# Performance work log

Hardware: AMD Instinct MI355X
Metric: run time of the kernel (lower is better)

## Reference

```python
import jax, jax.numpy as jnp
import numpy as np

EMBED = 1024
HEAD = 64
BLOCK = 2048
B = 8


def setup_inputs() -> dict:
    key = jax.random.key(0)
    k1, k2, k3, k4 = jax.random.split(key, 4)
    inputs = jax.random.normal(k1, (B, BLOCK, EMBED), dtype=jnp.float32)
    s = 1.0 / np.sqrt(EMBED)
    Wk = jax.random.normal(k2, (EMBED, HEAD), dtype=jnp.float32) * s
    Wq = jax.random.normal(k3, (EMBED, HEAD), dtype=jnp.float32) * s
    Wv = jax.random.normal(k4, (EMBED, HEAD), dtype=jnp.float32) * s
    return {"inputs": inputs, "Wk": Wk, "Wq": Wq, "Wv": Wv}


def reference(inputs, Wk, Wq, Wv):
    # inputs: [B, T, E]; projections (bias-free Linear)
    k = inputs @ Wk  # [B, T, H]
    q = inputs @ Wq  # [B, T, H]
    v = inputs @ Wv  # [B, T, H]
    # Faithful to source: wei = k @ q^T (NOT q @ k^T)
    wei = jnp.einsum("bth,bsh->bts", k, q) * (HEAD ** -0.5)  # [B, T, T]
    T = inputs.shape[1]
    causal = jnp.tril(jnp.ones((T, T), dtype=bool))
    wei = jnp.where(causal, wei, -jnp.inf)
    wei = jax.nn.softmax(wei, axis=-1)
    out = jnp.einsum("bts,bsh->bth", wei, v)  # [B, T, H]
    return out
```

## Files before the change

### kernel.cpp

```cpp
#include <hip/hip_runtime.h>
#include <hip/hip_bf16.h>
#include <stdint.h>


typedef __attribute__((ext_vector_type(4))) float f32x4;
typedef __attribute__((ext_vector_type(4))) short s16x4;
typedef __attribute__((ext_vector_type(8))) short s16x8;
typedef __attribute__((ext_vector_type(2))) unsigned int u32x2;
typedef __attribute__((ext_vector_type(4))) unsigned int u32x4;

__device__ __forceinline__ unsigned bf16pack(float a, float b){
    unsigned ua = __builtin_bit_cast(unsigned, a);
    unsigned ub = __builtin_bit_cast(unsigned, b);
    return ((ua + 0x8000u) >> 16) | ((ub + 0x8000u) & 0xffff0000u);
}
__device__ __forceinline__ unsigned short bf16one(float a){
    return (unsigned short)((__builtin_bit_cast(unsigned, a) + 0x8000u) >> 16);
}
__device__ __forceinline__ void gload16(const void* g, unsigned short* l){
    __builtin_amdgcn_global_load_lds((const __attribute__((address_space(1))) unsigned int*)g,
                                     (__attribute__((address_space(3))) unsigned int*)l, 16, 0, 0);
}

__global__ __launch_bounds__(256) void wprep_kernel(const float* __restrict__ Wk,
                                                    const float* __restrict__ Wq,
                                                    const float* __restrict__ Wv,
                                                    unsigned short* __restrict__ WT){
    __shared__ float lw[1024][8];
    int w = blockIdx.x, n0 = blockIdx.y * 8, tid = threadIdx.x;
    const float* src = (w == 0) ? Wk : (w == 1) ? Wq : Wv;
    float scale = (w == 0) ? 0.18033688011112042f : 1.0f;
    for (int it = 0; it < 8; ++it){
        int idx = it * 256 + tid;
        int k = idx >> 1, half = idx & 1;
        f32x4 v = *(const f32x4*)(src + k * 64 + n0 + half * 4);
        *(f32x4*)&lw[k][half * 4] = v;
    }
    __syncthreads();
    int n = tid >> 5, kc = (tid & 31) * 32;
    unsigned short* dst = WT + (size_t)((w * 64 + n0 + n) * 1024 + kc);
    #pragma unroll
    for (int c = 0; c < 4; c++){
        s16x8 v;
        #pragma unroll
        for (int e = 0; e < 8; e++)
            v[e] = (short)bf16one(lw[kc + c * 8 + e][n] * scale);
        *(s16x8*)(dst + c * 8) = v;
    }
}

__global__ __launch_bounds__(256) void proj_kernel(const float* __restrict__ x,
                                                   const unsigned short* __restrict__ WT,
                                                   unsigned short* __restrict__ kb,
                                                   unsigned short* __restrict__ qb,
                                                   unsigned short* __restrict__ vT){
    __shared__ unsigned short smem[32768];
    int tid = threadIdx.x; int l = tid & 63; int w = tid >> 6;
    int lr = l & 15, lg = l >> 4;
    int row0 = blockIdx.x * 32;
    int b = row0 >> 11, t0 = row0 & 2047;
    const float* xbase = x + (size_t)row0 * 1024;

    auto stage = [&](int k0, int buf){
        #pragma unroll
        for (int t = 0; t < 2; t++){
            int i = w * 2 + t;
            int r = i * 4 + (l >> 4);
            int c = l & 15;
            gload16(xbase + (size_t)r * 1024 + k0 + ((c ^ ((r & 7) << 1)) * 4),
                    smem + buf * 4096 + i * 512);
        }
        #pragma unroll
        for (int u = 0; u < 6; u++){
            int i = w * 6 + u;
            int r = i * 8 + (l >> 3);
            int c = l & 7;
            gload16(WT + (size_t)r * 1024 + k0 + ((c ^ (r & 7)) * 8),
                    smem + 8192 + buf * 12288 + i * 512);
        }
    };

    f32x4 acc[2][3] = {};
    stage(0, 0);
    __syncthreads();
    int cur = 0;
    for (int k0 = 0; k0 < 1024; k0 += 64){
        int kn = (k0 + 64 < 1024) ? (k0 + 64) : 960;
        stage(kn, cur ^ 1);
        s16x8 af[2][2];
        #pragma unroll
        for (int mf = 0; mf < 2; mf++){
            int r = mf * 16 + lr;
            const unsigned short* xrow = smem + cur * 4096 + r * 128;
            #pragma unroll
            for (int kc = 0; kc < 2; kc++){
                int c0 = (kc * 8 + lg * 2) ^ ((r & 7) << 1);
                f32x4 v0 = *(const f32x4*)(xrow + c0 * 8);
                f32x4 v1 = *(const f32x4*)(xrow + c0 * 8 + 8);
                u32x4 pk;
                pk[0] = bf16pack(v0[0], v0[1]); pk[1] = bf16pack(v0[2], v0[3]);
                pk[2] = bf16pack(v1[0], v1[1]); pk[3] = bf16pack(v1[2], v1[3]);
                af[mf][kc] = __builtin_bit_cast(s16x8, pk);
            }
        }
        #pragma unroll
        for (int nn = 0; nn < 3; nn++){
            int r = (w * 3 + nn) * 16 + lr;
            const unsigned short* wrow = smem + 8192 + cur * 12288 + r * 64;
            s16x8 b0 = *(const s16x8*)(wrow + ((lg       ^ (r & 7)) * 8));
            s16x8 b1 = *(const s16x8*)(wrow + (((4 + lg) ^ (r & 7)) * 8));
            acc[0][nn] = __builtin_amdgcn_mfma_f32_16x16x32_bf16(af[0][0], b0, acc[0][nn], 0, 0, 0);
            acc[0][nn] = __builtin_amdgcn_mfma_f32_16x16x32_bf16(af[0][1], b1, acc[0][nn], 0, 0, 0);
            acc[1][nn] = __builtin_amdgcn_mfma_f32_16x16x32_bf16(af[1][0], b0, acc[1][nn], 0, 0, 0);
            acc[1][nn] = __builtin_amdgcn_mfma_f32_16x16x32_bf16(af[1][1], b1, acc[1][nn], 0, 0, 0);
        }
        __syncthreads();
        cur ^= 1;
    }
    #pragma unroll
    for (int mf = 0; mf < 2; mf++)
        #pragma unroll
        for (int nn = 0; nn < 3; nn++){
            int col = (w * 3 + nn) * 16 + lr;
            int row = mf * 16 + lg * 4;
            #pragma unroll
            for (int r = 0; r < 4; r++)
                smem[(row + r) * 200 + col] = bf16one(acc[mf][nn][r]);
        }
    __syncthreads();
    {
        int r2 = tid >> 3, c2 = (tid & 7) * 16;
        const unsigned short* srowp = smem + r2 * 200 + c2;
        unsigned short* dst = (c2 < 64)
            ? kb + (size_t)(b * 2048 + t0 + r2) * 64 + c2
            : qb + (size_t)(b * 2048 + t0 + r2) * 64 + (c2 - 64);
        *(s16x8*)(dst)     = *(const s16x8*)(srowp);
        *(s16x8*)(dst + 8) = *(const s16x8*)(srowp + 8);
        int h = tid >> 2, q3 = tid & 3;
        s16x8 vv;
        #pragma unroll
        for (int e = 0; e < 8; e++)
            vv[e] = smem[(q3 * 8 + e) * 200 + 128 + h];
        *(s16x8*)(vT + (size_t)(b * 64 + h) * 2048 + t0 + q3 * 8) = vv;
    }
}

template<int NS>
__global__ __launch_bounds__(256) void attn_part_kernel(const unsigned short* __restrict__ kb,
                                                        const unsigned short* __restrict__ qb,
                                                        const unsigned short* __restrict__ vT,
                                                        float* __restrict__ out,
                                                        float* __restrict__ accp,
                                                        float* __restrict__ ml){
    __shared__ unsigned short Klds[2][64 * 64];
    __shared__ unsigned short Vlds[2][64 * 64];
    int tid = threadIdx.x; int l = tid & 63; int w = tid >> 6;
    int lr = l & 15, lg = l >> 4;
    int bx = blockIdx.x;
    int b = bx & 7;
    int r9 = bx >> 3;
    int bt = 31 - (r9 / NS);
    int strip = r9 % NS;
    int t0 = bt * 64;
    int tw = t0 + w * 16;
    const unsigned short* fqp = kb + (size_t)(b * 2048 + tw + lr) * 64 + lg * 8;
    s16x8 fq0 = *(const s16x8*)(fqp);
    s16x8 fq1 = *(const s16x8*)(fqp + 32);
    const unsigned short* qbb = qb + (size_t)b * 2048 * 64;
    const unsigned short* vbb = vT + (size_t)b * 64 * 2048;

    int srhi = l >> 3;
    int schk = l & 7;
    f32x4 acc[4] = {};
    float mrun = -3.0e38f, lrun = 0.0f;

    {
        int s0 = strip * 64;
        #pragma unroll
        for (int t = 0; t < 2; t++){
            int ti = w * 2 + t;
            int row = ti * 8 + srhi;
            gload16(qbb + (size_t)(s0 + row) * 64 + ((schk ^ (row & 7)) * 8), &Klds[0][ti * 512]);
            gload16(vbb + (size_t)row * 2048 + s0 + ((schk ^ (row & 7)) * 8), &Vlds[0][ti * 512]);
        }
    }
    __syncthreads();
    int cur = 0;
    for (int c = strip; c <= bt; c += NS){
        int nc = (c + NS <= bt) ? (c + NS) : c;
        int ns0 = nc * 64;
        #pragma unroll
        for (int t = 0; t < 2; t++){
            int ti = w * 2 + t;
            int row = ti * 8 + srhi;
            gload16(qbb + (size_t)(ns0 + row) * 64 + ((schk ^ (row & 7)) * 8), &Klds[cur ^ 1][ti * 512]);
            gload16(vbb + (size_t)row * 2048 + ns0 + ((schk ^ (row & 7)) * 8), &Vlds[cur ^ 1][ti * 512]);
        }
        f32x4 Cs[4];
        #pragma unroll
        for (int n = 0; n < 4; n++){
            int r = n * 16 + lr;
            const unsigned short* ka = &Klds[cur][r * 64];
            s16x8 k0 = *(const s16x8*)(ka + ((lg       ^ (r & 7)) * 8));
            s16x8 k1 = *(const s16x8*)(ka + (((4 + lg) ^ (r & 7)) * 8));
            f32x4 z = {};
            z     = __builtin_amdgcn_mfma_f32_16x16x32_bf16(k0, fq0, z, 0, 0, 0);
            Cs[n] = __builtin_amdgcn_mfma_f32_16x16x32_bf16(k1, fq1, z, 0, 0, 0);
        }
        if (c == bt){
            #pragma unroll
            for (int n = 0; n < 4; n++)
                #pragma unroll
                for (int r = 0; r < 4; r++)
                    if (n * 16 + lg * 4 + r > w * 16 + lr) Cs[n][r] = -3.0e38f;
        }
        float pm = -3.0e38f;
        #pragma unroll
        for (int n = 0; n < 4; n++)
            #pragma unroll
            for (int r = 0; r < 4; r++) pm = fmaxf(pm, Cs[n][r]);
        pm = fmaxf(pm, __shfl_xor(pm, 16));
        pm = fmaxf(pm, __shfl_xor(pm, 32));
        float mnew;
        if (__all(pm <= mrun + 8.0f)){
            mnew = mrun;
        } else {
            mnew = fmaxf(mrun, pm);
            float scl = exp2f(mrun - mnew);
            lrun *= scl;
            #pragma unroll
            for (int h16 = 0; h16 < 4; h16++) acc[h16] *= scl;
        }
        float p[4][4]; float ps = 0.0f;
        #pragma unroll
        for (int n = 0; n < 4; n++)
            #pragma unroll
            for (int r = 0; r < 4; r++){ float e = exp2f(Cs[n][r] - mnew); p[n][r] = e; ps += e; }
        ps += __shfl_xor(ps, 16);
        ps += __shfl_xor(ps, 32);
        lrun += ps;
        mrun = mnew;
        s16x4 pb[4];
        #pragma unroll
        for (int n = 0; n < 4; n++){
            u32x2 t; t[0] = bf16pack(p[n][0], p[n][1]); t[1] = bf16pack(p[n][2], p[n][3]);
            pb[n] = __builtin_bit_cast(s16x4, t);
        }
        #pragma unroll
        for (int h16 = 0; h16 < 4; h16++){
            int r = h16 * 16 + lr;
            const unsigned short* va = &Vlds[cur][r * 64];
            #pragma unroll
            for (int sl = 0; sl < 4; sl++){
                s16x4 fv = *(const s16x4*)(va + (((sl * 2 + (lg >> 1)) ^ (r & 7)) * 8) + (lg & 1) * 4);
                acc[h16] = __builtin_amdgcn_mfma_f32_16x16x16bf16_1k(fv, pb[sl], acc[h16], 0, 0, 0);
            }
        }
        __syncthreads();
        cur ^= 1;
    }
    float* accdst = (strip == 0) ? out : (accp + (size_t)(strip - 1) * (8 * 2048 * 64));
    #pragma unroll
    for (int h16 = 0; h16 < 4; h16++)
        *(f32x4*)(accdst + (size_t)(b * 2048 + tw + lr) * 64 + h16 * 16 + lg * 4) = acc[h16];
    if (lg == 0){
        int idx = ((strip * 8 + b) * 32 + bt) * 64 + w * 16 + lr;
        ml[idx * 2]     = mrun;
        ml[idx * 2 + 1] = lrun;
    }
}

template<int NS>
__global__ __launch_bounds__(256) void attn_merge_kernel(const float* __restrict__ accp,
                                                         const float* __restrict__ ml,
                                                         float* __restrict__ out){
    int bx = blockIdx.x;
    int b = bx & 7, bt = bx >> 3;
    int tid = threadIdx.x;
    int row = tid >> 2, cg = (tid & 3) * 16;
    float m[NS], lv[NS];
    float mg = -3.0e38f;
    #pragma unroll
    for (int s = 0; s < NS; s++){
        int idx = (((s * 8 + b) * 32 + bt) * 64 + row) * 2;
        m[s] = ml[idx]; lv[s] = ml[idx + 1];
        mg = fmaxf(mg, m[s]);
    }
    float wt[NS]; float lt = 0.0f;
    #pragma unroll
    for (int s = 0; s < NS; s++){ wt[s] = exp2f(m[s] - mg); lt += lv[s] * wt[s]; }
    float inv = 1.0f / lt;
    size_t base = (size_t)(b * 2048 + bt * 64 + row) * 64 + cg;
    #pragma unroll
    for (int g = 0; g < 4; g++){
        f32x4 o = (*(const f32x4*)(out + base + g * 4)) * wt[0];
        #pragma unroll
        for (int s = 1; s < NS; s++)
            o += (*(const f32x4*)(accp + (size_t)(s - 1) * (8 * 2048 * 64) + base + g * 4)) * wt[s];
        o *= inv;
        *(f32x4*)(out + base + g * 4) = o;
    }
}

__global__ __launch_bounds__(256) void attn_kernel(const unsigned short* __restrict__ kb,
                                                   const unsigned short* __restrict__ qb,
                                                   const unsigned short* __restrict__ vT,
                                                   float* __restrict__ out){
    __shared__ unsigned short Klds[2][64 * 64];
    __shared__ unsigned short Vlds[2][64 * 64];
    int tid = threadIdx.x; int l = tid & 63; int w = tid >> 6;
    int lr = l & 15, lg = l >> 4;
    int bx = blockIdx.x;
    int b = bx & 7;
    int bt = bx >> 3;
    int t0 = bt * 64;
    int tw = t0 + w * 16;
    const unsigned short* fqp = kb + (size_t)(b * 2048 + tw + lr) * 64 + lg * 8;
    s16x8 fq0 = *(const s16x8*)(fqp);
    s16x8 fq1 = *(const s16x8*)(fqp + 32);
    const unsigned short* qbb = qb + (size_t)b * 2048 * 64;
    const unsigned short* vbb = vT + (size_t)b * 64 * 2048;
    int srhi = l >> 3;
    int schk = l & 7;
    f32x4 acc[4] = {};
    float mrun = -3.0e38f, lrun = 0.0f;
    #pragma unroll
    for (int t = 0; t < 2; t++){
        int ti = w * 2 + t;
        int row = ti * 8 + srhi;
        gload16(qbb + (size_t)row * 64 + ((schk ^ (row & 7)) * 8), &Klds[0][ti * 512]);
        gload16(vbb + (size_t)row * 2048 + ((schk ^ (row & 7)) * 8), &Vlds[0][ti * 512]);
    }
    __syncthreads();
    int cur = 0;
    for (int c = 0; c <= bt; ++c){
        int nc = (c + 1 <= bt) ? (c + 1) : bt;
        int ns0 = nc * 64;
        #pragma unroll
        for (int t = 0; t < 2; t++){
            int ti = w * 2 + t;
            int row = ti * 8 + srhi;
            gload16(qbb + (size_t)(ns0 + row) * 64 + ((schk ^ (row & 7)) * 8), &Klds[cur ^ 1][ti * 512]);
            gload16(vbb + (size_t)row * 2048 + ns0 + ((schk ^ (row & 7)) * 8), &Vlds[cur ^ 1][ti * 512]);
        }
        f32x4 Cs[4];
        #pragma unroll
        for (int n = 0; n < 4; n++){
            int r = n * 16 + lr;
            const unsigned short* ka = &Klds[cur][r * 64];
            s16x8 k0 = *(const s16x8*)(ka + ((lg       ^ (r & 7)) * 8));
            s16x8 k1 = *(const s16x8*)(ka + (((4 + lg) ^ (r & 7)) * 8));
            f32x4 z = {};
            z     = __builtin_amdgcn_mfma_f32_16x16x32_bf16(k0, fq0, z, 0, 0, 0);
            Cs[n] = __builtin_amdgcn_mfma_f32_16x16x32_bf16(k1, fq1, z, 0, 0, 0);
        }
        if (c == bt){
            #pragma unroll
            for (int n = 0; n < 4; n++)
                #pragma unroll
                for (int r = 0; r < 4; r++)
                    if (n * 16 + lg * 4 + r > w * 16 + lr) Cs[n][r] = -3.0e38f;
        }
        float pm = -3.0e38f;
        #pragma unroll
        for (int n = 0; n < 4; n++)
            #pragma unroll
            for (int r = 0; r < 4; r++) pm = fmaxf(pm, Cs[n][r]);
        pm = fmaxf(pm, __shfl_xor(pm, 16));
        pm = fmaxf(pm, __shfl_xor(pm, 32));
        float mnew = fmaxf(mrun, pm);
        float scl = exp2f(mrun - mnew);
        float p[4][4]; float ps = 0.0f;
        #pragma unroll
        for (int n = 0; n < 4; n++)
            #pragma unroll
            for (int r = 0; r < 4; r++){ float e = exp2f(Cs[n][r] - mnew); p[n][r] = e; ps += e; }
        ps += __shfl_xor(ps, 16);
        ps += __shfl_xor(ps, 32);
        lrun = lrun * scl + ps;
        mrun = mnew;
        #pragma unroll
        for (int h16 = 0; h16 < 4; h16++) acc[h16] *= scl;
        s16x4 pb[4];
        #pragma unroll
        for (int n = 0; n < 4; n++){
            u32x2 t; t[0] = bf16pack(p[n][0], p[n][1]); t[1] = bf16pack(p[n][2], p[n][3]);
            pb[n] = __builtin_bit_cast(s16x4, t);
        }
        #pragma unroll
        for (int h16 = 0; h16 < 4; h16++){
            int r = h16 * 16 + lr;
            const unsigned short* va = &Vlds[cur][r * 64];
            #pragma unroll
            for (int sl = 0; sl < 4; sl++){
                s16x4 fv = *(const s16x4*)(va + (((sl * 2 + (lg >> 1)) ^ (r & 7)) * 8) + (lg & 1) * 4);
                acc[h16] = __builtin_amdgcn_mfma_f32_16x16x16bf16_1k(fv, pb[sl], acc[h16], 0, 0, 0);
            }
        }
        __syncthreads();
        cur ^= 1;
    }
    float inv = 1.0f / lrun;
    #pragma unroll
    for (int h16 = 0; h16 < 4; h16++){
        f32x4 o = acc[h16] * inv;
        *(f32x4*)(out + (size_t)(b * 2048 + tw + lr) * 64 + h16 * 16 + lg * 4) = o;
    }
}

extern "C" void kernel_launch(void* const* d_in, const int* in_sizes, int n_in,
                              void* d_out, int out_size, void* d_ws, size_t ws_size,
                              hipStream_t stream) {
    const float* x  = (const float*)d_in[0];
    const float* Wk = (const float*)d_in[1];
    const float* Wq = (const float*)d_in[2];
    const float* Wv = (const float*)d_in[3];
    float* out = (float*)d_out;
    char* ws = (char*)d_ws;
    if (ws_size < (size_t)7 * 1024 * 1024) return;
    unsigned short* WT = (unsigned short*)(ws);
    unsigned short* kb = (unsigned short*)(ws + (1u << 20));
    unsigned short* qb = (unsigned short*)(ws + (3u << 20));
    unsigned short* vT = (unsigned short*)(ws + (5u << 20));
    hipLaunchKernelGGL(wprep_kernel, dim3(3, 8), dim3(256), 0, stream, Wk, Wq, Wv, WT);
    hipLaunchKernelGGL(proj_kernel, dim3(512), dim3(256), 0, stream, x, WT, kb, qb, vT);
    if (ws_size >= (size_t)20 * 1024 * 1024){
        float* accp = (float*)(ws + ((size_t)7 << 20));
        float* ml   = (float*)(ws + ((size_t)19 << 20));
        hipLaunchKernelGGL((attn_part_kernel<4>), dim3(1024), dim3(256), 0, stream,
                           kb, qb, vT, out, accp, ml);
        hipLaunchKernelGGL((attn_merge_kernel<4>), dim3(256), dim3(256), 0, stream,
                           accp, ml, out);
    } else if (ws_size >= (size_t)12 * 1024 * 1024){
        float* accp = (float*)(ws + ((size_t)7 << 20));
        float* ml   = (float*)(ws + ((size_t)11 << 20));
        hipLaunchKernelGGL((attn_part_kernel<2>), dim3(512), dim3(256), 0, stream,
                           kb, qb, vT, out, accp, ml);
        hipLaunchKernelGGL((attn_merge_kernel<2>), dim3(256), dim3(256), 0, stream,
                           accp, ml, out);
    } else {
        hipLaunchKernelGGL(attn_kernel, dim3(256), dim3(256), 0, stream, kb, qb, vT, out);
    }
}
```

Measured before the change: 50.04 us.

## Triple-buffer x tiles and use partial vmcnt waits in projection GEMM

Splits staging of the activation and weight tiles so the fp32 x tiles are prefetched two steps ahead in a triple buffer, while weights keep a double buffer. The full __syncthreads is replaced by s_waitcnt vmcnt(2) plus a raw barrier, so the two most recent x loads can stay in flight across iterations. The aim is to hide global-to-LDS latency for the large x stream in the memory-bound projection. It costs more LDS per block and relies on manual vmcnt accounting, which is fragile if the compiler reorders or adds memory ops.

```diff
diff --git a/kernel.cpp b/kernel.cpp
--- a/kernel.cpp
+++ b/kernel.cpp
@@ -54,14 +54,14 @@
                                                    unsigned short* __restrict__ kb,
                                                    unsigned short* __restrict__ qb,
                                                    unsigned short* __restrict__ vT){
-    __shared__ unsigned short smem[32768];
+    __shared__ unsigned short smem[36864];
     int tid = threadIdx.x; int l = tid & 63; int w = tid >> 6;
     int lr = l & 15, lg = l >> 4;
     int row0 = blockIdx.x * 32;
     int b = row0 >> 11, t0 = row0 & 2047;
     const float* xbase = x + (size_t)row0 * 1024;
 
-    auto stage = [&](int k0, int buf){
+    auto stage_x = [&](int k0, int buf){
         #pragma unroll
         for (int t = 0; t < 2; t++){
             int i = w * 2 + t;
@@ -70,28 +70,39 @@
             gload16(xbase + (size_t)r * 1024 + k0 + ((c ^ ((r & 7) << 1)) * 4),
                     smem + buf * 4096 + i * 512);
         }
+    };
+    auto stage_w = [&](int k0, int buf){
         #pragma unroll
         for (int u = 0; u < 6; u++){
             int i = w * 6 + u;
             int r = i * 8 + (l >> 3);
             int c = l & 7;
             gload16(WT + (size_t)r * 1024 + k0 + ((c ^ (r & 7)) * 8),
-                    smem + 8192 + buf * 12288 + i * 512);
+                    smem + 12288 + buf * 12288 + i * 512);
         }
     };
 
     f32x4 acc[2][3] = {};
-    stage(0, 0);
-    __syncthreads();
-    int cur = 0;
-    for (int k0 = 0; k0 < 1024; k0 += 64){
-        int kn = (k0 + 64 < 1024) ? (k0 + 64) : 960;
-        stage(kn, cur ^ 1);
+    stage_x(0, 0);
+    stage_w(0, 0);
+    stage_x(64, 1);
+    asm volatile("s_waitcnt vmcnt(2)" ::: "memory");
+    __builtin_amdgcn_s_barrier();
+    asm volatile("" ::: "memory");
+
+    for (int i = 0; i < 16; ++i){
+        int k0 = i * 64;
+        int kw = (k0 + 64  < 1024) ? (k0 + 64)  : 960;
+        int kx = (k0 + 128 < 1024) ? (k0 + 128) : 960;
+        stage_w(kw, (i + 1) & 1);
+        stage_x(kx, (i + 2) % 3);
+        const unsigned short* xb = smem + (i % 3) * 4096;
+        const unsigned short* wb = smem + 12288 + (i & 1) * 12288;
         s16x8 af[2][2];
         #pragma unroll
         for (int mf = 0; mf < 2; mf++){
             int r = mf * 16 + lr;
-            const unsigned short* xrow = smem + cur * 4096 + r * 128;
+            const unsigned short* xrow = xb + r * 128;
             #pragma unroll
             for (int kc = 0; kc < 2; kc++){
                 int c0 = (kc * 8 + lg * 2) ^ ((r & 7) << 1);
@@ -106,7 +117,7 @@
         #pragma unroll
         for (int nn = 0; nn < 3; nn++){
             int r = (w * 3 + nn) * 16 + lr;
-            const unsigned short* wrow = smem + 8192 + cur * 12288 + r * 64;
+            const unsigned short* wrow = wb + r * 64;
             s16x8 b0 = *(const s16x8*)(wrow + ((lg       ^ (r & 7)) * 8));
             s16x8 b1 = *(const s16x8*)(wrow + (((4 + lg) ^ (r & 7)) * 8));
             acc[0][nn] = __builtin_amdgcn_mfma_f32_16x16x32_bf16(af[0][0], b0, acc[0][nn], 0, 0, 0);
@@ -114,9 +125,14 @@
             acc[1][nn] = __builtin_amdgcn_mfma_f32_16x16x32_bf16(af[1][0], b0, acc[1][nn], 0, 0, 0);
             acc[1][nn] = __builtin_amdgcn_mfma_f32_16x16x32_bf16(af[1][1], b1, acc[1][nn], 0, 0, 0);
         }
-        __syncthreads();
-        cur ^= 1;
-    }
+        asm volatile("s_waitcnt vmcnt(2)" ::: "memory");
+        __builtin_amdgcn_s_barrier();
+        asm volatile("" ::: "memory");
+    }
+    asm volatile("s_waitcnt vmcnt(0)" ::: "memory");
+    __builtin_amdgcn_s_barrier();
+    asm volatile("" ::: "memory");
+
     #pragma unroll
     for (int mf = 0; mf < 2; mf++)
         #pragma unroll
```

Result: slower. 53.04 us (+6.0%).
